# Performance work log

Hardware: AMD Instinct MI355X
Metric: run time of the kernel (lower is better)

Reference implementation:

```python
import jax, jax.numpy as jnp
import numpy as np

N = 100_000
E = 1_600_000
F_IN = 128
HID = 64
HEADS = 2
HC = HID // HEADS  # 32 per-head channels
EPS = 1e-5
NEG_SLOPE = 0.2


def _layer_norm(x, g, b):
    mu = jnp.mean(x, axis=-1, keepdims=True)
    var = jnp.mean(jnp.square(x - mu), axis=-1, keepdims=True)
    return (x - mu) * jax.lax.rsqrt(var + EPS) * g + b


def _batch_norm(x, g, b):
    # training-mode batch statistics over the node axis (biased variance)
    mu = jnp.mean(x, axis=0, keepdims=True)
    var = jnp.mean(jnp.square(x - mu), axis=0, keepdims=True)
    return (x - mu) * jax.lax.rsqrt(var + EPS) * g + b


def _gcn_conv(x, src, dst, W, bias, n):
    # PyG GCNConv: self-loops already included in (src, dst); symmetric norm
    deg = jax.ops.segment_sum(jnp.ones_like(src, dtype=x.dtype), dst, num_segments=n)
    dinv = jnp.where(deg > 0, jax.lax.rsqrt(deg), 0.0)
    norm = dinv[src] * dinv[dst]                      # [E2]
    xw = x @ W                                        # [N, out]
    msg = xw[src] * norm[:, None]                     # gather + scale
    out = jax.ops.segment_sum(msg, dst, num_segments=n)
    return out + bias


def _gat_conv(x, src, dst, W, att_src, att_dst, bias, n):
    # PyG GATConv, heads=HEADS, concat=True (self-loops included in src/dst)
    xw = (x @ W).reshape(n, HEADS, HC)                # [N, H, C]
    a_s = jnp.sum(xw * att_src, axis=-1)              # [N, H]
    a_d = jnp.sum(xw * att_dst, axis=-1)              # [N, H]
    e = jax.nn.leaky_relu(a_s[src] + a_d[dst], NEG_SLOPE)  # [E2, H]
    m = jax.ops.segment_max(e, dst, num_segments=n)   # per-target max for stability
    e = jnp.exp(e - m[dst])
    denom = jax.ops.segment_sum(e, dst, num_segments=n)
    alpha = e / (denom[dst] + 1e-16)                  # neighborhood softmax
    out = jax.ops.segment_sum(xw[src] * alpha[:, :, None], dst, num_segments=n)
    return out.reshape(n, HEADS * HC) + bias


def setup_inputs() -> dict:
    key = jax.random.key(0)
    ks = jax.random.split(key, 20)
    f32 = jnp.float32
    d = {}
    d["accessibility_features"] = jax.random.normal(ks[0], (N, F_IN), dtype=f32)
    d["edge_index"] = jax.random.randint(ks[1], (2, E), 0, N, dtype=jnp.int64)
    # LayerNorm
    d["ln_g"] = jnp.ones((F_IN,), f32); d["ln_b"] = jnp.zeros((F_IN,), f32)
    # feature encoder
    d["enc_w1"] = jax.random.normal(ks[2], (F_IN, HID), f32) * (2.0 / (F_IN + HID)) ** 0.5
    d["enc_b1"] = jnp.zeros((HID,), f32)
    d["enc_w2"] = jax.random.normal(ks[3], (HID, HID), f32) * (1.0 / HID) ** 0.5
    d["enc_b2"] = jnp.zeros((HID,), f32)
    # GCN 1
    d["gcn1_w"] = jax.random.normal(ks[4], (HID, HID), f32) * (1.0 / HID) ** 0.5
    d["gcn1_b"] = jnp.zeros((HID,), f32)
    d["bn1_g"] = jnp.ones((HID,), f32); d["bn1_b"] = jnp.zeros((HID,), f32)
    # GAT
    d["gat_w"] = jax.random.normal(ks[5], (HID, HEADS * HC), f32) * (1.0 / HID) ** 0.5
    d["gat_as"] = jax.random.normal(ks[6], (HEADS, HC), f32) * 0.1
    d["gat_ad"] = jax.random.normal(ks[7], (HEADS, HC), f32) * 0.1
    d["gat_b"] = jnp.zeros((HEADS * HC,), f32)
    d["bn2_g"] = jnp.ones((HID,), f32); d["bn2_b"] = jnp.zeros((HID,), f32)
    # GCN 2 -> hidden//2
    d["gcn2_w"] = jax.random.normal(ks[8], (HID, HID // 2), f32) * (2.0 / (HID + HID // 2)) ** 0.5
    d["gcn2_b"] = jnp.zeros((HID // 2,), f32)
    d["bn3_g"] = jnp.ones((HID // 2,), f32); d["bn3_b"] = jnp.zeros((HID // 2,), f32)
    # prediction head
    d["pred_w1"] = jax.random.normal(ks[9], (HID // 2, HID // 4), f32) * (2.0 / (HID // 2 + HID // 4)) ** 0.5
    d["pred_b1"] = jnp.zeros((HID // 4,), f32)
    d["pred_w2"] = jax.random.normal(ks[10], (HID // 4, 1), f32) * (2.0 / (HID // 4 + 1)) ** 0.5
    d["pred_b2"] = jnp.zeros((1,), f32)
    return d


def reference(accessibility_features, edge_index, ln_g, ln_b, enc_w1, enc_b1,
              enc_w2, enc_b2, gcn1_w, gcn1_b, bn1_g, bn1_b, gat_w, gat_as,
              gat_ad, gat_b, bn2_g, bn2_b, gcn2_w, gcn2_b, bn3_g, bn3_b,
              pred_w1, pred_b1, pred_w2, pred_b2):
    n = accessibility_features.shape[0]
    loops = jnp.arange(n, dtype=edge_index.dtype)
    src = jnp.concatenate([edge_index[0], loops])   # add self-loops once
    dst = jnp.concatenate([edge_index[1], loops])

    x = _layer_norm(accessibility_features, ln_g, ln_b)
    x = jax.nn.relu(x @ enc_w1 + enc_b1)            # dropout = identity (eval)
    x = jax.nn.relu(x @ enc_w2 + enc_b2)

    x = _gcn_conv(x, src, dst, gcn1_w, gcn1_b, n)
    x = jax.nn.relu(_batch_norm(x, bn1_g, bn1_b))

    xa = _gat_conv(x, src, dst, gat_w, gat_as, gat_ad, gat_b, n)
    xa = jax.nn.relu(_batch_norm(xa, bn2_g, bn2_b))

    x = _gcn_conv(xa, src, dst, gcn2_w, gcn2_b, n)
    x = jax.nn.relu(_batch_norm(x, bn3_g, bn3_b))

    h = jax.nn.relu(x @ pred_w1 + pred_b1)
    svi = jax.nn.sigmoid((h @ pred_w2 + pred_b2).squeeze(-1))
    return svi
```

## Files before the change

### kernel.cpp

```cpp
#include <hip/hip_runtime.h>
#include <math.h>

#define F_IN 128
#define HID  64
#define EPS  1e-5f
#define NSLOPE 0.2f
#define BSH 9
#define MAXBUK 1024
#define EPB 4096
#define SPB 4096

__device__ __forceinline__ float lrelu(float x) { return x > 0.f ? x : NSLOPE * x; }

__device__ __forceinline__ unsigned short f2bf(float f) {
  unsigned u = __float_as_uint(f);
  return (unsigned short)((u + 0x7FFF + ((u >> 16) & 1)) >> 16);
}
__device__ __forceinline__ float bf2f(unsigned short b) {
  return __uint_as_float((unsigned)b << 16);
}


__global__ __launch_bounds__(256) void k_buk_count(const int* __restrict__ ei,
                                                   int* __restrict__ bukcnt, int E, int nbuk) {
  __shared__ int lc[MAXBUK];
  for (int k = threadIdx.x; k < nbuk; k += 256) lc[k] = 0;
  __syncthreads();
  int base = blockIdx.x * EPB, end = min(E, base + EPB);
  for (int t = base + threadIdx.x; t < end; t += 256) atomicAdd(&lc[ei[E + t] >> BSH], 1);
  __syncthreads();
  for (int k = threadIdx.x; k < nbuk; k += 256)
    if (lc[k]) atomicAdd(&bukcnt[k], lc[k]);
}

__global__ void k_buk_scan(const int* __restrict__ bukcnt, int* __restrict__ bukbase, int nbuk) {
  __shared__ int l[MAXBUK + 1];
  for (int k = threadIdx.x; k < nbuk; k += blockDim.x) l[k] = bukcnt[k];
  __syncthreads();
  if (threadIdx.x == 0) {
    int r = 0;
    for (int k = 0; k < nbuk; ++k) { int t = l[k]; l[k] = r; r += t; }
    l[nbuk] = r;
  }
  __syncthreads();
  for (int k = threadIdx.x; k <= nbuk; k += blockDim.x) bukbase[k] = l[k];
}

__global__ __launch_bounds__(256) void k_buk_scatter(const int* __restrict__ ei,
                                                     const int* __restrict__ bukbase,
                                                     int* __restrict__ bukcur,
                                                     int2* __restrict__ pairs, int E, int nbuk) {
  __shared__ int lc[MAXBUK];
  __shared__ int lbase[MAXBUK];
  for (int k = threadIdx.x; k < nbuk; k += 256) lc[k] = 0;
  __syncthreads();
  int base = blockIdx.x * EPB, end = min(E, base + EPB);
  for (int t = base + threadIdx.x; t < end; t += 256) atomicAdd(&lc[ei[E + t] >> BSH], 1);
  __syncthreads();
  for (int k = threadIdx.x; k < nbuk; k += 256) {
    int c = lc[k];
    lbase[k] = c ? atomicAdd(&bukcur[k], c) : 0;
  }
  __syncthreads();
  for (int k = threadIdx.x; k < nbuk; k += 256) lc[k] = 0;
  __syncthreads();
  for (int t = base + threadIdx.x; t < end; t += 256) {
    int s = ei[t], d = ei[E + t];
    int b = d >> BSH;
    int o = atomicAdd(&lc[b], 1);
    pairs[bukbase[b] + lbase[b] + o] = make_int2(s, d);
  }
}

__global__ __launch_bounds__(256) void k_buk_deg(const int2* __restrict__ pairs,
                                                 const int* __restrict__ bukbase,
                                                 int* __restrict__ ideg, int N) {
  __shared__ int ldeg[1 << BSH];
  int b = blockIdx.x;
  for (int k = threadIdx.x; k < (1 << BSH); k += 256) ldeg[k] = 0;
  __syncthreads();
  int s0 = bukbase[b], s1 = bukbase[b + 1], nb = b << BSH;
  for (int t = s0 + threadIdx.x; t < s1; t += 256) atomicAdd(&ldeg[pairs[t].y - nb], 1);
  __syncthreads();
  for (int k = threadIdx.x; k < (1 << BSH); k += 256) {
    int node = nb + k;
    if (node < N) ideg[node] = ldeg[k];
  }
}

__global__ __launch_bounds__(256) void k_scan_sums(const int* __restrict__ ideg,
                                                   int* __restrict__ bsum, int N) {
  __shared__ int red[256];
  int base = blockIdx.x * SPB + threadIdx.x * 16;
  int s = 0;
#pragma unroll
  for (int j = 0; j < 16; ++j) { int i = base + j; if (i < N) s += ideg[i] + 1; }
  red[threadIdx.x] = s;
  __syncthreads();
  for (int o = 128; o; o >>= 1) {
    if (threadIdx.x < o) red[threadIdx.x] += red[threadIdx.x + o];
    __syncthreads();
  }
  if (threadIdx.x == 0) bsum[blockIdx.x] = red[0];
}

__global__ void k_scan_tops(int* __restrict__ bsum, int nb) {
  __shared__ int l[MAXBUK];
  for (int k = threadIdx.x; k < nb; k += blockDim.x) l[k] = bsum[k];
  __syncthreads();
  if (threadIdx.x == 0) {
    int r = 0;
    for (int k = 0; k < nb; ++k) { int t = l[k]; l[k] = r; r += t; }
  }
  __syncthreads();
  for (int k = threadIdx.x; k < nb; k += blockDim.x) bsum[k] = l[k];
}

__global__ __launch_bounds__(256) void k_scan_apply(const int* __restrict__ ideg,
                                                    const int* __restrict__ bsum,
                                                    int* __restrict__ rowstart,
                                                    float* __restrict__ dinv,
                                                    int* __restrict__ csr, int N) {
  __shared__ int pre[256];
  int base = blockIdx.x * SPB + threadIdx.x * 16;
  int deg[16];
  int s = 0;
#pragma unroll
  for (int j = 0; j < 16; ++j) {
    int i = base + j;
    int d = (i < N) ? ideg[i] + 1 : 0;
    deg[j] = d; s += d;
  }
  pre[threadIdx.x] = s;
  __syncthreads();
  for (int o = 1; o < 256; o <<= 1) {
    int v = (threadIdx.x >= o) ? pre[threadIdx.x - o] : 0;
    __syncthreads();
    pre[threadIdx.x] += v;
    __syncthreads();
  }
  int off = bsum[blockIdx.x] + pre[threadIdx.x] - s;
#pragma unroll
  for (int j = 0; j < 16; ++j) {
    int i = base + j;
    if (i < N) {
      rowstart[i] = off;
      dinv[i] = rsqrtf((float)deg[j]);
      csr[off] = i;
      off += deg[j];
    }
  }
}

__global__ __launch_bounds__(256) void k_buk_fill(const int2* __restrict__ pairs,
                                                  const int* __restrict__ bukbase,
                                                  const int* __restrict__ rowstart,
                                                  int* __restrict__ csr) {
  __shared__ int lcur[1 << BSH];
  int b = blockIdx.x;
  for (int k = threadIdx.x; k < (1 << BSH); k += 256) lcur[k] = 0;
  __syncthreads();
  int s0 = bukbase[b], s1 = bukbase[b + 1], nb = b << BSH;
  for (int t = s0 + threadIdx.x; t < s1; t += 256) {
    int2 pr = pairs[t];
    int o = atomicAdd(&lcur[pr.y - nb], 1);
    csr[rowstart[pr.y] + 1 + o] = pr.x;
  }
}

__global__ void k_precomp(const float* __restrict__ w1, const float* __restrict__ ln_g,
                          const float* __restrict__ ln_b, const float* __restrict__ b1,
                          float* __restrict__ w1g, float* __restrict__ c1,
                          float* __restrict__ cb) {
  int j = threadIdx.x;
  float c1v = 0.f, cbv = 0.f;
  for (int k = 0; k < F_IN; ++k) {
    float w = w1[k * HID + j];
    float wg = ln_g[k] * w;
    w1g[k * HID + j] = wg;
    c1v += wg;
    cbv += ln_b[k] * w;
  }
  c1[j] = c1v;
  cb[j] = cbv + b1[j];
}

__global__ __launch_bounds__(256) void k_enc(
    const float* __restrict__ x, const float* __restrict__ w1g,
    const float* __restrict__ c1, const float* __restrict__ cb,
    const float* __restrict__ w2, const float* __restrict__ b2,
    float* __restrict__ out, int N) {
  __shared__ float shl[256 * 65];
  int i = blockIdx.x * 256 + threadIdx.x;
  if (i >= N) return;
  const float4* xr = (const float4*)(x + (size_t)i * F_IN);
  float acc[HID];
#pragma unroll
  for (int j = 0; j < HID; ++j) acc[j] = 0.f;
  float s = 0.f, q = 0.f;
#pragma unroll 1
  for (int c = 0; c < F_IN / 4; ++c) {
    float4 xv = xr[c];
    s += xv.x + xv.y + xv.z + xv.w;
    q += xv.x * xv.x + xv.y * xv.y + xv.z * xv.z + xv.w * xv.w;
    const float* wr = w1g + c * 4 * HID;
#pragma unroll
    for (int e = 0; e < 4; ++e) {
      float xe = (e == 0) ? xv.x : (e == 1) ? xv.y : (e == 2) ? xv.z : xv.w;
      const float4* w4 = (const float4*)(wr + e * HID);
#pragma unroll
      for (int j4 = 0; j4 < HID / 4; ++j4) {
        float4 wv = w4[j4];
        acc[j4 * 4 + 0] += xe * wv.x;
        acc[j4 * 4 + 1] += xe * wv.y;
        acc[j4 * 4 + 2] += xe * wv.z;
        acc[j4 * 4 + 3] += xe * wv.w;
      }
    }
  }
  float mu = s * (1.f / F_IN);
  float var = q * (1.f / F_IN) - mu * mu;
  float rs = rsqrtf(var + EPS);
  int base = threadIdx.x * 65;
#pragma unroll
  for (int j = 0; j < HID; ++j)
    shl[base + j] = fmaxf(rs * (acc[j] - mu * c1[j]) + cb[j], 0.f);
  float acc2[HID];
#pragma unroll
  for (int j = 0; j < HID; ++j) acc2[j] = b2[j];
#pragma unroll 4
  for (int j = 0; j < HID; ++j) {
    float hj = shl[base + j];
    const float4* w4 = (const float4*)(w2 + j * HID);
#pragma unroll
    for (int c4 = 0; c4 < HID / 4; ++c4) {
      float4 wv = w4[c4];
      acc2[c4 * 4 + 0] += hj * wv.x;
      acc2[c4 * 4 + 1] += hj * wv.y;
      acc2[c4 * 4 + 2] += hj * wv.z;
      acc2[c4 * 4 + 3] += hj * wv.w;
    }
  }
  float4* o4 = (float4*)(out + (size_t)i * HID);
#pragma unroll
  for (int c4 = 0; c4 < HID / 4; ++c4)
    o4[c4] = make_float4(fmaxf(acc2[c4 * 4 + 0], 0.f), fmaxf(acc2[c4 * 4 + 1], 0.f),
                         fmaxf(acc2[c4 * 4 + 2], 0.f), fmaxf(acc2[c4 * 4 + 3], 0.f));
}

template <int FOUT, bool GAT, bool BNIN>
__global__ __launch_bounds__(256) void k_gemm_reg(
    const float* __restrict__ x, const float* __restrict__ w,
    const float* __restrict__ stats,
    const float* __restrict__ atts, const float* __restrict__ atd,
    unsigned short* __restrict__ out, float* __restrict__ a_s, float* __restrict__ a_d, int N) {
  int i = blockIdx.x * 256 + threadIdx.x;
  if (i >= N) return;
  const float4* xr = (const float4*)(x + (size_t)i * HID);
  float acc[FOUT];
#pragma unroll
  for (int j = 0; j < FOUT; ++j) acc[j] = 0.f;
#pragma unroll 1
  for (int c = 0; c < HID / 4; ++c) {
    float4 xv = xr[c];
    if (BNIN) {
      xv.x = fmaxf(xv.x * stats[c * 4 + 0] + stats[HID + c * 4 + 0], 0.f);
      xv.y = fmaxf(xv.y * stats[c * 4 + 1] + stats[HID + c * 4 + 1], 0.f);
      xv.z = fmaxf(xv.z * stats[c * 4 + 2] + stats[HID + c * 4 + 2], 0.f);
      xv.w = fmaxf(xv.w * stats[c * 4 + 3] + stats[HID + c * 4 + 3], 0.f);
    }
    const float* wr = w + c * 4 * FOUT;
#pragma unroll
    for (int e = 0; e < 4; ++e) {
      float xe = (e == 0) ? xv.x : (e == 1) ? xv.y : (e == 2) ? xv.z : xv.w;
      const float4* w4 = (const float4*)(wr + e * FOUT);
#pragma unroll
      for (int j4 = 0; j4 < FOUT / 4; ++j4) {
        float4 wv = w4[j4];
        acc[j4 * 4 + 0] += xe * wv.x;
        acc[j4 * 4 + 1] += xe * wv.y;
        acc[j4 * 4 + 2] += xe * wv.z;
        acc[j4 * 4 + 3] += xe * wv.w;
      }
    }
  }
  unsigned short* orow = out + (size_t)i * FOUT;
#pragma unroll
  for (int j8 = 0; j8 < FOUT / 8; ++j8) {
    uint4 pk;
    pk.x = ((unsigned)f2bf(acc[j8 * 8 + 1]) << 16) | f2bf(acc[j8 * 8 + 0]);
    pk.y = ((unsigned)f2bf(acc[j8 * 8 + 3]) << 16) | f2bf(acc[j8 * 8 + 2]);
    pk.z = ((unsigned)f2bf(acc[j8 * 8 + 5]) << 16) | f2bf(acc[j8 * 8 + 4]);
    pk.w = ((unsigned)f2bf(acc[j8 * 8 + 7]) << 16) | f2bf(acc[j8 * 8 + 6]);
    *(uint4*)(orow + j8 * 8) = pk;
  }
  if (GAT) {
    float s0 = 0.f, s1 = 0.f, d0 = 0.f, d1 = 0.f;
#pragma unroll
    for (int c = 0; c < 32; ++c) { s0 += acc[c] * atts[c]; d0 += acc[c] * atd[c]; }
#pragma unroll
    for (int c = 32; c < 64; ++c) { s1 += acc[c] * atts[c]; d1 += acc[c] * atd[c]; }
    a_s[i * 2] = s0; a_s[i * 2 + 1] = s1;
    a_d[i * 2] = d0; a_d[i * 2 + 1] = d1;
  }
}

__global__ __launch_bounds__(256) void k_gcn_pull64(
    const int* __restrict__ csr, const int* __restrict__ rowstart, const int* __restrict__ ideg,
    const float* __restrict__ dinv, const unsigned short* __restrict__ xw,
    float* __restrict__ out, int N) {
  int wave = threadIdx.x >> 6, lane = threadIdx.x & 63;
  int i = blockIdx.x * 4 + wave;
  if (i >= N) return;
  int row = rowstart[i], dg = ideg[i] + 1;
  float did = dinv[i];
  float acc = 0.f;
  for (int base = 0; base < dg; base += 64) {
    int cnt = min(64, dg - base);
    int sid = (lane < cnt) ? csr[row + base + lane] : 0;
    int n = 0;
    for (; n + 4 <= cnt; n += 4) {
      int s0 = __shfl(sid, n), s1 = __shfl(sid, n + 1);
      int s2 = __shfl(sid, n + 2), s3 = __shfl(sid, n + 3);
      acc += dinv[s0] * did * bf2f(xw[s0 * 64 + lane]) + dinv[s1] * did * bf2f(xw[s1 * 64 + lane]) +
             dinv[s2] * did * bf2f(xw[s2 * 64 + lane]) + dinv[s3] * did * bf2f(xw[s3 * 64 + lane]);
    }
    for (; n < cnt; ++n) {
      int s0 = __shfl(sid, n);
      acc += dinv[s0] * did * bf2f(xw[s0 * 64 + lane]);
    }
  }
  out[i * 64 + lane] = acc;
}

__global__ __launch_bounds__(256) void k_gcn_pull32(
    const int* __restrict__ csr, const int* __restrict__ rowstart, const int* __restrict__ ideg,
    const float* __restrict__ dinv, const unsigned short* __restrict__ xw,
    float* __restrict__ out, int N) {
  int wave = threadIdx.x >> 6, lane = threadIdx.x & 63;
  int half = lane >> 5, lf = lane & 31;
  int i = (blockIdx.x * 4 + wave) * 2 + half;
  if (i >= N) return;
  int row = rowstart[i], dg = ideg[i] + 1;
  float did = dinv[i];
  float acc = 0.f;
  for (int base = 0; base < dg; base += 32) {
    int cnt = min(32, dg - base);
    int sid = (lf < cnt) ? csr[row + base + lf] : 0;
    int n = 0;
    for (; n + 2 <= cnt; n += 2) {
      int s0 = __shfl(sid, n, 32), s1 = __shfl(sid, n + 1, 32);
      acc += dinv[s0] * did * bf2f(xw[s0 * 32 + lf]) + dinv[s1] * did * bf2f(xw[s1 * 32 + lf]);
    }
    for (; n < cnt; ++n) {
      int s0 = __shfl(sid, n, 32);
      acc += dinv[s0] * did * bf2f(xw[s0 * 32 + lf]);
    }
  }
  out[i * 32 + lf] = acc;
}

__global__ __launch_bounds__(256) void k_gat_fused(
    const int* __restrict__ csr, const int* __restrict__ rowstart, const int* __restrict__ ideg,
    const float* __restrict__ a_s, const float* __restrict__ a_d,
    const unsigned short* __restrict__ xw, float* __restrict__ out, int N) {
  int wave = threadIdx.x >> 6, lane = threadIdx.x & 63;
  int i = blockIdx.x * 4 + wave;
  if (i >= N) return;
  int row = rowstart[i], dg = ideg[i] + 1;
  int h = lane >> 5;
  float ad0 = a_d[i * 2], ad1 = a_d[i * 2 + 1];
  float m0 = -1e30f, m1 = -1e30f, z0 = 0.f, z1 = 0.f, acc = 0.f;
  for (int base = 0; base < dg; base += 64) {
    int cnt = min(64, dg - base);
    int sid = (lane < cnt) ? csr[row + base + lane] : 0;
    float e0 = -1e30f, e1 = -1e30f;
    if (lane < cnt) {
      e0 = lrelu(a_s[sid * 2] + ad0);
      e1 = lrelu(a_s[sid * 2 + 1] + ad1);
    }
    float cm0 = e0, cm1 = e1;
#pragma unroll
    for (int o = 32; o; o >>= 1) {
      cm0 = fmaxf(cm0, __shfl_xor(cm0, o));
      cm1 = fmaxf(cm1, __shfl_xor(cm1, o));
    }
    float nm0 = fmaxf(m0, cm0), nm1 = fmaxf(m1, cm1);
    float r0 = __expf(m0 - nm0), r1 = __expf(m1 - nm1);
    z0 *= r0; z1 *= r1;
    acc *= (h == 0) ? r0 : r1;
    m0 = nm0; m1 = nm1;
    float p0 = (lane < cnt) ? __expf(e0 - m0) : 0.f;
    float p1 = (lane < cnt) ? __expf(e1 - m1) : 0.f;
    float s0 = p0, s1 = p1;
#pragma unroll
    for (int o = 32; o; o >>= 1) { s0 += __shfl_xor(s0, o); s1 += __shfl_xor(s1, o); }
    z0 += s0; z1 += s1;
    int n = 0;
    for (; n + 2 <= cnt; n += 2) {
      int v0 = __shfl(sid, n), v1 = __shfl(sid, n + 1);
      float pa0 = __shfl(p0, n), pb0 = __shfl(p1, n);
      float pa1 = __shfl(p0, n + 1), pb1 = __shfl(p1, n + 1);
      float al0 = (h == 0) ? pa0 : pb0;
      float al1 = (h == 0) ? pa1 : pb1;
      acc += al0 * bf2f(xw[v0 * HID + lane]) + al1 * bf2f(xw[v1 * HID + lane]);
    }
    for (; n < cnt; ++n) {
      int v0 = __shfl(sid, n);
      float pa0 = __shfl(p0, n), pb0 = __shfl(p1, n);
      float al0 = (h == 0) ? pa0 : pb0;
      acc += al0 * bf2f(xw[v0 * HID + lane]);
    }
  }
  float zh = (h == 0) ? z0 : z1;
  out[i * HID + lane] = acc / (zh + 1e-16f);
}

template <int F>
__global__ __launch_bounds__(256) void k_bn_reduce(const float* __restrict__ x,
                                                   float* __restrict__ partials, int N) {
  __shared__ float sS[F], sQ[F];
  int tid = threadIdx.x;
  int t = blockIdx.x * 256 + tid;
  int stride = gridDim.x * 256;
  int total4 = N * F / 4;
  int f0 = (t * 4) % F;
  float s0 = 0, s1 = 0, s2 = 0, s3 = 0, q0 = 0, q1 = 0, q2 = 0, q3 = 0;
  for (int c = t; c < total4; c += stride) {
    float4 v = ((const float4*)x)[c];
    s0 += v.x; q0 += v.x * v.x;
    s1 += v.y; q1 += v.y * v.y;
    s2 += v.z; q2 += v.z * v.z;
    s3 += v.w; q3 += v.w * v.w;
  }
  if (tid < F) { sS[tid] = 0.f; sQ[tid] = 0.f; }
  __syncthreads();
  atomicAdd(&sS[f0], s0);     atomicAdd(&sQ[f0], q0);
  atomicAdd(&sS[f0 + 1], s1); atomicAdd(&sQ[f0 + 1], q1);
  atomicAdd(&sS[f0 + 2], s2); atomicAdd(&sQ[f0 + 2], q2);
  atomicAdd(&sS[f0 + 3], s3); atomicAdd(&sQ[f0 + 3], q3);
  __syncthreads();
  if (tid < F) {
    partials[blockIdx.x * 2 * F + tid]     = sS[tid];
    partials[blockIdx.x * 2 * F + F + tid] = sQ[tid];
  }
}

template <int F>
__global__ __launch_bounds__(1024) void k_bn_finalize(
    const float* __restrict__ partials, int nblk,
    float* __restrict__ stats, const float* __restrict__ g,
    const float* __restrict__ b, int N) {
  const int TF = 2 * F;
  const int NGRP = 1024 / TF;
  __shared__ float sh[1024];
  int tid = threadIdx.x;
  int f = tid % TF;
  int grp = tid / TF;
  float s = 0.f;
  for (int k = grp; k < nblk; k += NGRP) s += partials[(size_t)k * TF + f];
  sh[tid] = s;
  __syncthreads();
  for (int off = NGRP / 2; off > 0; off >>= 1) {
    if (grp < off) sh[tid] += sh[tid + off * TF];
    __syncthreads();
  }
  if (tid < F) {
    float S = sh[tid], Q = sh[F + tid];
    float mu = S / (float)N;
    float var = Q / (float)N - mu * mu;
    float sc = rsqrtf(var + EPS) * g[tid];
    stats[tid] = sc;
    stats[F + tid] = b[tid] - mu * sc;
  }
}

__global__ __launch_bounds__(256) void k_pred(
    const float* __restrict__ x, const float* __restrict__ stats,
    const float* __restrict__ w1, const float* __restrict__ b1,
    const float* __restrict__ w2, const float* __restrict__ b2,
    float* __restrict__ out, int N) {
  int i = blockIdx.x * 256 + threadIdx.x;
  if (i >= N) return;
  const float4* xr = (const float4*)(x + (size_t)i * 32);
  float acc[16];
#pragma unroll
  for (int j = 0; j < 16; ++j) acc[j] = b1[j];
#pragma unroll 1
  for (int c = 0; c < 8; ++c) {
    float4 xv = xr[c];
    xv.x = fmaxf(xv.x * stats[c * 4 + 0] + stats[32 + c * 4 + 0], 0.f);
    xv.y = fmaxf(xv.y * stats[c * 4 + 1] + stats[32 + c * 4 + 1], 0.f);
    xv.z = fmaxf(xv.z * stats[c * 4 + 2] + stats[32 + c * 4 + 2], 0.f);
    xv.w = fmaxf(xv.w * stats[c * 4 + 3] + stats[32 + c * 4 + 3], 0.f);
    const float* wr = w1 + c * 4 * 16;
#pragma unroll
    for (int e = 0; e < 4; ++e) {
      float xe = (e == 0) ? xv.x : (e == 1) ? xv.y : (e == 2) ? xv.z : xv.w;
      const float4* w4 = (const float4*)(wr + e * 16);
#pragma unroll
      for (int j4 = 0; j4 < 4; ++j4) {
        float4 wv = w4[j4];
        acc[j4 * 4 + 0] += xe * wv.x;
        acc[j4 * 4 + 1] += xe * wv.y;
        acc[j4 * 4 + 2] += xe * wv.z;
        acc[j4 * 4 + 3] += xe * wv.w;
      }
    }
  }
  float z = b2[0];
#pragma unroll
  for (int j = 0; j < 16; ++j) z += fmaxf(acc[j], 0.f) * w2[j];
  out[i] = 1.f / (1.f + __expf(-z));
}

extern "C" void kernel_launch(void* const* d_in, const int* in_sizes, int n_in,
                              void* d_out, int out_size, void* d_ws, size_t ws_size,
                              hipStream_t stream) {
  const float* x_in  = (const float*)d_in[0];
  const int*   ei    = (const int*)d_in[1];
  const float* ln_g  = (const float*)d_in[2];
  const float* ln_b  = (const float*)d_in[3];
  const float* enc_w1 = (const float*)d_in[4];
  const float* enc_b1 = (const float*)d_in[5];
  const float* enc_w2 = (const float*)d_in[6];
  const float* enc_b2 = (const float*)d_in[7];
  const float* gcn1_w = (const float*)d_in[8];
  const float* bn1_g = (const float*)d_in[10];
  const float* bn1_b = (const float*)d_in[11];
  const float* gat_w  = (const float*)d_in[12];
  const float* gat_as = (const float*)d_in[13];
  const float* gat_ad = (const float*)d_in[14];
  const float* bn2_g = (const float*)d_in[16];
  const float* bn2_b = (const float*)d_in[17];
  const float* gcn2_w = (const float*)d_in[18];
  const float* bn3_g = (const float*)d_in[20];
  const float* bn3_b = (const float*)d_in[21];
  const float* pw1 = (const float*)d_in[22];
  const float* pb1 = (const float*)d_in[23];
  const float* pw2 = (const float*)d_in[24];
  const float* pb2 = (const float*)d_in[25];
  float* out = (float*)d_out;

  int N = in_sizes[0] / F_IN;
  int E = in_sizes[1] / 2;
  int nbuk = (N + (1 << BSH) - 1) >> BSH;

  const int NBLK_BN = 512;

  char* p = (char*)d_ws;
  auto alloc = [&](size_t bytes) { char* r = p; p += (bytes + 255) & ~(size_t)255; return (void*)r; };
  float* h     = (float*)alloc((size_t)N * 64 * 4);
  unsigned short* xw = (unsigned short*)alloc((size_t)N * 64 * 2);
  float* agg   = (float*)alloc((size_t)N * 64 * 4);
  float* as_   = (float*)alloc((size_t)N * 2 * 4);
  float* ad_   = (float*)alloc((size_t)N * 2 * 4);
  float* dinv  = (float*)alloc((size_t)N * 4);
  float* stats = (float*)alloc(2 * 64 * 4);
  float* parts = (float*)alloc((size_t)NBLK_BN * 2 * 64 * 4);
  float* w1g   = (float*)alloc((size_t)F_IN * HID * 4);
  float* c1    = (float*)alloc(HID * 4);
  float* cb    = (float*)alloc(HID * 4);
  int* ideg    = (int*)alloc((size_t)N * 4);
  int* rowst   = (int*)alloc((size_t)N * 4);
  int* csr     = (int*)alloc((size_t)(N + E) * 4);
  int* bukcnt  = (int*)alloc((size_t)MAXBUK * 4);
  int* bukbase = (int*)alloc((size_t)(MAXBUK + 1) * 4);
  int* bukcur  = (int*)alloc((size_t)MAXBUK * 4);
  int* bsum    = (int*)alloc((size_t)MAXBUK * 4);
  int2* pairs  = (int2*)h;

  hipMemsetAsync(bukcnt, 0, (size_t)nbuk * 4, stream);
  hipMemsetAsync(bukcur, 0, (size_t)nbuk * 4, stream);

  int EB = (E + EPB - 1) / EPB;
  int SB = (N + SPB - 1) / SPB;
  int NB = (N + 255) / 256;
  int NB4 = (N + 3) / 4;
  int NB8 = (N + 7) / 8;

  k_buk_count<<<EB, 256, 0, stream>>>(ei, bukcnt, E, nbuk);
  k_buk_scan<<<1, 256, 0, stream>>>(bukcnt, bukbase, nbuk);
  k_buk_scatter<<<EB, 256, 0, stream>>>(ei, bukbase, bukcur, pairs, E, nbuk);
  k_buk_deg<<<nbuk, 256, 0, stream>>>(pairs, bukbase, ideg, N);
  k_scan_sums<<<SB, 256, 0, stream>>>(ideg, bsum, N);
  k_scan_tops<<<1, 256, 0, stream>>>(bsum, SB);
  k_scan_apply<<<SB, 256, 0, stream>>>(ideg, bsum, rowst, dinv, csr, N);
  k_buk_fill<<<nbuk, 256, 0, stream>>>(pairs, bukbase, rowst, csr);

  k_precomp<<<1, 64, 0, stream>>>(enc_w1, ln_g, ln_b, enc_b1, w1g, c1, cb);
  k_enc<<<NB, 256, 0, stream>>>(x_in, w1g, c1, cb, enc_w2, enc_b2, h, N);

  k_gemm_reg<64, false, false><<<NB, 256, 0, stream>>>(h, gcn1_w, nullptr, nullptr, nullptr,
                                                       xw, nullptr, nullptr, N);
  k_gcn_pull64<<<NB4, 256, 0, stream>>>(csr, rowst, ideg, dinv, xw, agg, N);
  k_bn_reduce<64><<<NBLK_BN, 256, 0, stream>>>(agg, parts, N);
  k_bn_finalize<64><<<1, 1024, 0, stream>>>(parts, NBLK_BN, stats, bn1_g, bn1_b, N);

  k_gemm_reg<64, true, true><<<NB, 256, 0, stream>>>(agg, gat_w, stats, gat_as, gat_ad,
                                                     xw, as_, ad_, N);
  k_gat_fused<<<NB4, 256, 0, stream>>>(csr, rowst, ideg, as_, ad_, xw, h, N);
  k_bn_reduce<64><<<NBLK_BN, 256, 0, stream>>>(h, parts, N);
  k_bn_finalize<64><<<1, 1024, 0, stream>>>(parts, NBLK_BN, stats, bn2_g, bn2_b, N);

  k_gemm_reg<32, false, true><<<NB, 256, 0, stream>>>(h, gcn2_w, stats, nullptr, nullptr,
                                                      xw, nullptr, nullptr, N);
  k_gcn_pull32<<<NB8, 256, 0, stream>>>(csr, rowst, ideg, dinv, xw, agg, N);
  k_bn_reduce<32><<<NBLK_BN, 256, 0, stream>>>(agg, parts, N);
  k_bn_finalize<32><<<1, 1024, 0, stream>>>(parts, NBLK_BN, stats, bn3_g, bn3_b, N);

  k_pred<<<NB, 256, 0, stream>>>(agg, stats, pw1, pb1, pw2, pb2, out, N);
}
```

Before: 549.4 us.

## Fuse BatchNorm statistics into aggregation kernels with grid-stride persistent blocks

The three aggregation kernels (GCN pull 64/32 and fused GAT) now use a fixed-size grid with a grid-stride loop. Each kernel accumulates per-feature sum and sum-of-squares in shared memory via atomics and writes per-block partials, so the separate k_bn_reduce passes that re-read the full activation arrays are removed. The GAT inner loop is also unrolled by four with two accumulators to expose more memory-level parallelism. The cost is shared-memory atomic contention on every node, plus fewer resident blocks, which could hurt latency hiding for the irregular gathers.

Result: slower. 778.3 us (+41.7%).

```diff
diff --git a/kernel.cpp b/kernel.cpp
--- a/kernel.cpp
+++ b/kernel.cpp
@@ -9,6 +9,8 @@
 #define MAXBUK 1024
 #define EPB 4096
 #define SPB 4096
+#define GRID_P64 2048
+#define GRID_P32 1024
 
 __device__ __forceinline__ float lrelu(float x) { return x > 0.f ? x : NSLOPE * x; }
 
@@ -19,7 +21,6 @@
 __device__ __forceinline__ float bf2f(unsigned short b) {
   return __uint_as_float((unsigned)b << 16);
 }
-
 
 __global__ __launch_bounds__(256) void k_buk_count(const int* __restrict__ ei,
                                                    int* __restrict__ bukcnt, int E, int nbuk) {
@@ -308,141 +309,159 @@
 __global__ __launch_bounds__(256) void k_gcn_pull64(
     const int* __restrict__ csr, const int* __restrict__ rowstart, const int* __restrict__ ideg,
     const float* __restrict__ dinv, const unsigned short* __restrict__ xw,
-    float* __restrict__ out, int N) {
+    float* __restrict__ out, float* __restrict__ partials, int N) {
+  __shared__ float sS[64], sQ[64];
   int wave = threadIdx.x >> 6, lane = threadIdx.x & 63;
-  int i = blockIdx.x * 4 + wave;
-  if (i >= N) return;
-  int row = rowstart[i], dg = ideg[i] + 1;
-  float did = dinv[i];
-  float acc = 0.f;
-  for (int base = 0; base < dg; base += 64) {
-    int cnt = min(64, dg - base);
-    int sid = (lane < cnt) ? csr[row + base + lane] : 0;
-    int n = 0;
-    for (; n + 4 <= cnt; n += 4) {
-      int s0 = __shfl(sid, n), s1 = __shfl(sid, n + 1);
-      int s2 = __shfl(sid, n + 2), s3 = __shfl(sid, n + 3);
-      acc += dinv[s0] * did * bf2f(xw[s0 * 64 + lane]) + dinv[s1] * did * bf2f(xw[s1 * 64 + lane]) +
-             dinv[s2] * did * bf2f(xw[s2 * 64 + lane]) + dinv[s3] * did * bf2f(xw[s3 * 64 + lane]);
-    }
-    for (; n < cnt; ++n) {
-      int s0 = __shfl(sid, n);
-      acc += dinv[s0] * did * bf2f(xw[s0 * 64 + lane]);
-    }
-  }
-  out[i * 64 + lane] = acc;
+  if (threadIdx.x < 64) { sS[threadIdx.x] = 0.f; sQ[threadIdx.x] = 0.f; }
+  __syncthreads();
+  for (int ib = blockIdx.x; ib * 4 < N; ib += gridDim.x) {
+    int i = ib * 4 + wave;
+    if (i < N) {
+      int row = rowstart[i], dg = ideg[i] + 1;
+      float did = dinv[i];
+      float acc = 0.f;
+      for (int base = 0; base < dg; base += 64) {
+        int cnt = min(64, dg - base);
+        int sid = (lane < cnt) ? csr[row + base + lane] : 0;
+        int n = 0;
+        for (; n + 4 <= cnt; n += 4) {
+          int s0 = __shfl(sid, n), s1 = __shfl(sid, n + 1);
+          int s2 = __shfl(sid, n + 2), s3 = __shfl(sid, n + 3);
+          acc += dinv[s0] * did * bf2f(xw[s0 * 64 + lane]) + dinv[s1] * did * bf2f(xw[s1 * 64 + lane]) +
+                 dinv[s2] * did * bf2f(xw[s2 * 64 + lane]) + dinv[s3] * did * bf2f(xw[s3 * 64 + lane]);
+        }
+        for (; n < cnt; ++n) {
+          int s0 = __shfl(sid, n);
+          acc += dinv[s0] * did * bf2f(xw[s0 * 64 + lane]);
+        }
+      }
+      out[i * 64 + lane] = acc;
+      atomicAdd(&sS[lane], acc);
+      atomicAdd(&sQ[lane], acc * acc);
+    }
+  }
+  __syncthreads();
+  if (threadIdx.x < 64) {
+    partials[blockIdx.x * 128 + threadIdx.x] = sS[threadIdx.x];
+    partials[blockIdx.x * 128 + 64 + threadIdx.x] = sQ[threadIdx.x];
+  }
 }
 
 __global__ __launch_bounds__(256) void k_gcn_pull32(
     const int* __restrict__ csr, const int* __restrict__ rowstart, const int* __restrict__ ideg,
     const float* __restrict__ dinv, const unsigned short* __restrict__ xw,
-    float* __restrict__ out, int N) {
+    float* __restrict__ out, float* __restrict__ partials, int N) {
+  __shared__ float sS[32], sQ[32];
   int wave = threadIdx.x >> 6, lane = threadIdx.x & 63;
   int half = lane >> 5, lf = lane & 31;
-  int i = (blockIdx.x * 4 + wave) * 2 + half;
-  if (i >= N) return;
-  int row = rowstart[i], dg = ideg[i] + 1;
-  float did = dinv[i];
-  float acc = 0.f;
-  for (int base = 0; base < dg; base += 32) {
-    int cnt = min(32, dg - base);
-    int sid = (lf < cnt) ? csr[row + base + lf] : 0;
-    int n = 0;
-    for (; n + 2 <= cnt; n += 2) {
-      int s0 = __shfl(sid, n, 32), s1 = __shfl(sid, n + 1, 32);
-      acc += dinv[s0] * did * bf2f(xw[s0 * 32 + lf]) + dinv[s1] * did * bf2f(xw[s1 * 32 + lf]);
-    }
-    for (; n < cnt; ++n) {
-      int s0 = __shfl(sid, n, 32);
-      acc += dinv[s0] * did * bf2f(xw[s0 * 32 + lf]);
-    }
-  }
-  out[i * 32 + lf] = acc;
+  if (threadIdx.x < 32) { sS[threadIdx.x] = 0.f; sQ[threadIdx.x] = 0.f; }
+  __syncthreads();
+  for (int ib = blockIdx.x; ib * 8 < N; ib += gridDim.x) {
+    int i = (ib * 4 + wave) * 2 + half;
+    if (i < N) {
+      int row = rowstart[i], dg = ideg[i] + 1;
+      float did = dinv[i];
+      float acc = 0.f;
+      for (int base = 0; base < dg; base += 32) {
+        int cnt = min(32, dg - base);
+        int sid = (lf < cnt) ? csr[row + base + lf] : 0;
+        int n = 0;
+        for (; n + 2 <= cnt; n += 2) {
+          int s0 = __shfl(sid, n, 32), s1 = __shfl(sid, n + 1, 32);
+          acc += dinv[s0] * did * bf2f(xw[s0 * 32 + lf]) + dinv[s1] * did * bf2f(xw[s1 * 32 + lf]);
+        }
+        for (; n < cnt; ++n) {
+          int s0 = __shfl(sid, n, 32);
+          acc += dinv[s0] * did * bf2f(xw[s0 * 32 + lf]);
+        }
+      }
+      out[i * 32 + lf] = acc;
+      atomicAdd(&sS[lf], acc);
+      atomicAdd(&sQ[lf], acc * acc);
+    }
+  }
+  __syncthreads();
+  if (threadIdx.x < 32) {
+    partials[blockIdx.x * 64 + threadIdx.x] = sS[threadIdx.x];
+    partials[blockIdx.x * 64 + 32 + threadIdx.x] = sQ[threadIdx.x];
+  }
 }
 
 __global__ __launch_bounds__(256) void k_gat_fused(
     const int* __restrict__ csr, const int* __restrict__ rowstart, const int* __restrict__ ideg,
     const float* __restrict__ a_s, const float* __restrict__ a_d,
-    const unsigned short* __restrict__ xw, float* __restrict__ out, int N) {
+    const unsigned short* __restrict__ xw, float* __restrict__ out,
+    float* __restrict__ partials, int N) {
+  __shared__ float sS[64], sQ[64];
   int wave = threadIdx.x >> 6, lane = threadIdx.x & 63;
-  int i = blockIdx.x * 4 + wave;
-  if (i >= N) return;
-  int row = rowstart[i], dg = ideg[i] + 1;
+  if (threadIdx.x < 64) { sS[threadIdx.x] = 0.f; sQ[threadIdx.x] = 0.f; }
+  __syncthreads();
   int h = lane >> 5;
-  float ad0 = a_d[i * 2], ad1 = a_d[i * 2 + 1];
-  float m0 = -1e30f, m1 = -1e30f, z0 = 0.f, z1 = 0.f, acc = 0.f;
-  for (int base = 0; base < dg; base += 64) {
-    int cnt = min(64, dg - base);
-    int sid = (lane < cnt) ? csr[row + base + lane] : 0;
-    float e0 = -1e30f, e1 = -1e30f;
-    if (lane < cnt) {
-      e0 = lrelu(a_s[sid * 2] + ad0);
-      e1 = lrelu(a_s[sid * 2 + 1] + ad1);
-    }
-    float cm0 = e0, cm1 = e1;
-#pragma unroll
-    for (int o = 32; o; o >>= 1) {
-      cm0 = fmaxf(cm0, __shfl_xor(cm0, o));
-      cm1 = fmaxf(cm1, __shfl_xor(cm1, o));
-    }
-    float nm0 = fmaxf(m0, cm0), nm1 = fmaxf(m1, cm1);
-    float r0 = __expf(m0 - nm0), r1 = __expf(m1 - nm1);
-    z0 *= r0; z1 *= r1;
-    acc *= (h == 0) ? r0 : r1;
-    m0 = nm0; m1 = nm1;
-    float p0 = (lane < cnt) ? __expf(e0 - m0) : 0.f;
-    float p1 = (lane < cnt) ? __expf(e1 - m1) : 0.f;
-    float s0 = p0, s1 = p1;
-#pragma unroll
-    for (int o = 32; o; o >>= 1) { s0 += __shfl_xor(s0, o); s1 += __shfl_xor(s1, o); }
-    z0 += s0; z1 += s1;
-    int n = 0;
-    for (; n + 2 <= cnt; n += 2) {
-      int v0 = __shfl(sid, n), v1 = __shfl(sid, n + 1);
-      float pa0 = __shfl(p0, n), pb0 = __shfl(p1, n);
-      float pa1 = __shfl(p0, n + 1), pb1 = __shfl(p1, n + 1);
-      float al0 = (h == 0) ? pa0 : pb0;
-      float al1 = (h == 0) ? pa1 : pb1;
-      acc += al0 * bf2f(xw[v0 * HID + lane]) + al1 * bf2f(xw[v1 * HID + lane]);
-    }
-    for (; n < cnt; ++n) {
-      int v0 = __shfl(sid, n);
-      float pa0 = __shfl(p0, n), pb0 = __shfl(p1, n);
-      float al0 = (h == 0) ? pa0 : pb0;
-      acc += al0 * bf2f(xw[v0 * HID + lane]);
-    }
-  }
-  float zh = (h == 0) ? z0 : z1;
-  out[i * HID + lane] = acc / (zh + 1e-16f);
-}
-
-template <int F>
-__global__ __launch_bounds__(256) void k_bn_reduce(const float* __restrict__ x,
-                                                   float* __restrict__ partials, int N) {
-  __shared__ float sS[F], sQ[F];
-  int tid = threadIdx.x;
-  int t = blockIdx.x * 256 + tid;
-  int stride = gridDim.x * 256;
-  int total4 = N * F / 4;
-  int f0 = (t * 4) % F;
-  float s0 = 0, s1 = 0, s2 = 0, s3 = 0, q0 = 0, q1 = 0, q2 = 0, q3 = 0;
-  for (int c = t; c < total4; c += stride) {
-    float4 v = ((const float4*)x)[c];
-    s0 += v.x; q0 += v.x * v.x;
-    s1 += v.y; q1 += v.y * v.y;
-    s2 += v.z; q2 += v.z * v.z;
-    s3 += v.w; q3 += v.w * v.w;
-  }
-  if (tid < F) { sS[tid] = 0.f; sQ[tid] = 0.f; }
-  __syncthreads();
-  atomicAdd(&sS[f0], s0);     atomicAdd(&sQ[f0], q0);
-  atomicAdd(&sS[f0 + 1], s1); atomicAdd(&sQ[f0 + 1], q1);
-  atomicAdd(&sS[f0 + 2], s2); atomicAdd(&sQ[f0 + 2], q2);
-  atomicAdd(&sS[f0 + 3], s3); atomicAdd(&sQ[f0 + 3], q3);
-  __syncthreads();
-  if (tid < F) {
-    partials[blockIdx.x * 2 * F + tid]     = sS[tid];
-    partials[blockIdx.x * 2 * F + F + tid] = sQ[tid];
+  for (int ib = blockIdx.x; ib * 4 < N; ib += gridDim.x) {
+    int i = ib * 4 + wave;
+    if (i < N) {
+      int row = rowstart[i], dg = ideg[i] + 1;
+      float ad0 = a_d[i * 2], ad1 = a_d[i * 2 + 1];
+      float m0 = -1e30f, m1 = -1e30f, z0 = 0.f, z1 = 0.f, accA = 0.f, accB = 0.f;
+      for (int base = 0; base < dg; base += 64) {
+        int cnt = min(64, dg - base);
+        int sid = (lane < cnt) ? csr[row + base + lane] : 0;
+        float e0 = -1e30f, e1 = -1e30f;
+        if (lane < cnt) {
+          e0 = lrelu(a_s[sid * 2] + ad0);
+          e1 = lrelu(a_s[sid * 2 + 1] + ad1);
+        }
+        float cm0 = e0, cm1 = e1;
+#pragma unroll
+        for (int o = 32; o; o >>= 1) {
+          cm0 = fmaxf(cm0, __shfl_xor(cm0, o));
+          cm1 = fmaxf(cm1, __shfl_xor(cm1, o));
+        }
+        float nm0 = fmaxf(m0, cm0), nm1 = fmaxf(m1, cm1);
+        float r0 = __expf(m0 - nm0), r1 = __expf(m1 - nm1);
+        z0 *= r0; z1 *= r1;
+        float rh = (h == 0) ? r0 : r1;
+        accA *= rh; accB *= rh;
+        m0 = nm0; m1 = nm1;
+        float p0 = (lane < cnt) ? __expf(e0 - m0) : 0.f;
+        float p1 = (lane < cnt) ? __expf(e1 - m1) : 0.f;
+        float s0 = p0, s1 = p1;
+#pragma unroll
+        for (int o = 32; o; o >>= 1) { s0 += __shfl_xor(s0, o); s1 += __shfl_xor(s1, o); }
+        z0 += s0; z1 += s1;
+        int n = 0;
+        for (; n + 4 <= cnt; n += 4) {
+          int v0 = __shfl(sid, n), v1 = __shfl(sid, n + 1);
+          int v2 = __shfl(sid, n + 2), v3 = __shfl(sid, n + 3);
+          float pa0 = __shfl(p0, n),     pb0 = __shfl(p1, n);
+          float pa1 = __shfl(p0, n + 1), pb1 = __shfl(p1, n + 1);
+          float pa2 = __shfl(p0, n + 2), pb2 = __shfl(p1, n + 2);
+          float pa3 = __shfl(p0, n + 3), pb3 = __shfl(p1, n + 3);
+          float al0 = (h == 0) ? pa0 : pb0;
+          float al1 = (h == 0) ? pa1 : pb1;
+          float al2 = (h == 0) ? pa2 : pb2;
+          float al3 = (h == 0) ? pa3 : pb3;
+          accA += al0 * bf2f(xw[v0 * HID + lane]) + al1 * bf2f(xw[v1 * HID + lane]);
+          accB += al2 * bf2f(xw[v2 * HID + lane]) + al3 * bf2f(xw[v3 * HID + lane]);
+        }
+        for (; n < cnt; ++n) {
+          int v0 = __shfl(sid, n);
+          float pa0 = __shfl(p0, n), pb0 = __shfl(p1, n);
+          float al0 = (h == 0) ? pa0 : pb0;
+          accA += al0 * bf2f(xw[v0 * HID + lane]);
+        }
+      }
+      float zh = (h == 0) ? z0 : z1;
+      float v = (accA + accB) / (zh + 1e-16f);
+      out[i * HID + lane] = v;
+      atomicAdd(&sS[lane], v);
+      atomicAdd(&sQ[lane], v * v);
+    }
+  }
+  __syncthreads();
+  if (threadIdx.x < 64) {
+    partials[blockIdx.x * 128 + threadIdx.x] = sS[threadIdx.x];
+    partials[blockIdx.x * 128 + 64 + threadIdx.x] = sQ[threadIdx.x];
   }
 }
 
@@ -546,8 +565,6 @@
   int E = in_sizes[1] / 2;
   int nbuk = (N + (1 << BSH) - 1) >> BSH;
 
-  const int NBLK_BN = 512;
-
   char* p = (char*)d_ws;
   auto alloc = [&](size_t bytes) { char* r = p; p += (bytes + 255) & ~(size_t)255; return (void*)r; };
   float* h     = (float*)alloc((size_t)N * 64 * 4);
@@ -557,7 +574,7 @@
   float* ad_   = (float*)alloc((size_t)N * 2 * 4);
   float* dinv  = (float*)alloc((size_t)N * 4);
   float* stats = (float*)alloc(2 * 64 * 4);
-  float* parts = (float*)alloc((size_t)NBLK_BN * 2 * 64 * 4);
+  float* parts = (float*)alloc((size_t)GRID_P64 * 2 * 64 * 4);
   float* w1g   = (float*)alloc((size_t)F_IN * HID * 4);
   float* c1    = (float*)alloc(HID * 4);
   float* cb    = (float*)alloc(HID * 4);
@@ -576,8 +593,8 @@
   int EB = (E + EPB - 1) / EPB;
   int SB = (N + SPB - 1) / SPB;
   int NB = (N + 255) / 256;
-  int NB4 = (N + 3) / 4;
-  int NB8 = (N + 7) / 8;
+  int GP64 = min(GRID_P64, (N + 3) / 4);
+  int GP32 = min(GRID_P32, (N + 7) / 8);
 
   k_buk_count<<<EB, 256, 0, stream>>>(ei, bukcnt, E, nbuk);
   k_buk_scan<<<1, 256, 0, stream>>>(bukcnt, bukbase, nbuk);
@@ -593,21 +610,18 @@
 
   k_gemm_reg<64, false, false><<<NB, 256, 0, stream>>>(h, gcn1_w, nullptr, nullptr, nullptr,
                                                        xw, nullptr, nullptr, N);
-  k_gcn_pull64<<<NB4, 256, 0, stream>>>(csr, rowst, ideg, dinv, xw, agg, N);
-  k_bn_reduce<64><<<NBLK_BN, 256, 0, stream>>>(agg, parts, N);
-  k_bn_finalize<64><<<1, 1024, 0, stream>>>(parts, NBLK_BN, stats, bn1_g, bn1_b, N);
+  k_gcn_pull64<<<GP64, 256, 0, stream>>>(csr, rowst, ideg, dinv, xw, agg, parts, N);
+  k_bn_finalize<64><<<1, 1024, 0, stream>>>(parts, GP64, stats, bn1_g, bn1_b, N);
 
   k_gemm_reg<64, true, true><<<NB, 256, 0, stream>>>(agg, gat_w, stats, gat_as, gat_ad,
                                                      xw, as_, ad_, N);
-  k_gat_fused<<<NB4, 256, 0, stream>>>(csr, rowst, ideg, as_, ad_, xw, h, N);
-  k_bn_reduce<64><<<NBLK_BN, 256, 0, stream>>>(h, parts, N);
-  k_bn_finalize<64><<<1, 1024, 0, stream>>>(parts, NBLK_BN, stats, bn2_g, bn2_b, N);
+  k_gat_fused<<<GP64, 256, 0, stream>>>(csr, rowst, ideg, as_, ad_, xw, h, parts, N);
+  k_bn_finalize<64><<<1, 1024, 0, stream>>>(parts, GP64, stats, bn2_g, bn2_b, N);
 
   k_gemm_reg<32, false, true><<<NB, 256, 0, stream>>>(h, gcn2_w, stats, nullptr, nullptr,
                                                       xw, nullptr, nullptr, N);
-  k_gcn_pull32<<<NB8, 256, 0, stream>>>(csr, rowst, ideg, dinv, xw, agg, N);
-  k_bn_reduce<32><<<NBLK_BN, 256, 0, stream>>>(agg, parts, N);
-  k_bn_finalize<32><<<1, 1024, 0, stream>>>(parts, NBLK_BN, stats, bn3_g, bn3_b, N);
+  k_gcn_pull32<<<GP32, 256, 0, stream>>>(csr, rowst, ideg, dinv, xw, agg, parts, N);
+  k_bn_finalize<32><<<1, 1024, 0, stream>>>(parts, GP32, stats, bn3_g, bn3_b, N);
 
   k_pred<<<NB, 256, 0, stream>>>(agg, stats, pw1, pb1, pw2, pb2, out, N);
 }
```
